# Kernel tuning notes

Measured on AMD Instinct MI355X. Metric: run time of the kernel, lower is better.

## Reference

```python
import jax, jax.numpy as jnp
import numpy as np

B, C, HIMG, WIMG = 32, 3, 512, 512


def setup_inputs() -> dict:
    key = jax.random.key(0)
    k1, k2, k3 = jax.random.split(key, 3)
    eye = jnp.eye(3, dtype=jnp.float32).reshape(1, 9)
    # near-identity homographies so inversion is well-conditioned
    H_pred = eye + 0.05 * jax.random.normal(k1, (B, 9), dtype=jnp.float32)
    H_true = eye + 0.05 * jax.random.normal(k2, (B, 9), dtype=jnp.float32)
    I = jax.random.normal(k3, (B, C, HIMG, WIMG), dtype=jnp.float32)
    return {"H_pred": H_pred, "H_true": H_true, "I": I}


def _build_perspective_grid(H_inv, height, width):
    # H_inv: [B,3,3] -> normalized sampling grid [B,height,width,2]
    xs = jnp.arange(width, dtype=jnp.float32)
    ys = jnp.arange(height, dtype=jnp.float32)
    gy, gx = jnp.meshgrid(ys, xs, indexing='ij')
    pts = jnp.stack([gx.ravel(), gy.ravel(), jnp.ones(height * width, dtype=jnp.float32)], axis=0)  # [3,N]
    new = jnp.einsum('bij,jn->bin', H_inv, pts)          # [B,3,N]
    new = new / new[:, 2:3, :]
    x_norm = 2.0 * new[:, 0] / (width - 1) - 1.0
    y_norm = 2.0 * new[:, 1] / (height - 1) - 1.0
    return jnp.stack([x_norm, y_norm], axis=-1).reshape(-1, height, width, 2)


def _grid_sample_bilinear_zeros(img, grid):
    # img: [B,C,H,W], grid: [B,H,W,2] in [-1,1]; align_corners=False, padding zeros
    Bn, Cn, Hn, Wn = img.shape
    x = ((grid[..., 0] + 1.0) * Wn - 1.0) * 0.5
    y = ((grid[..., 1] + 1.0) * Hn - 1.0) * 0.5
    x0 = jnp.floor(x); y0 = jnp.floor(y)
    x1 = x0 + 1.0;     y1 = y0 + 1.0
    wx1 = x - x0; wx0 = 1.0 - wx1
    wy1 = y - y0; wy0 = 1.0 - wy1

    def gather(xi, yi):
        valid = (xi >= 0) & (xi < Wn) & (yi >= 0) & (yi < Hn)
        xi_c = jnp.clip(xi, 0, Wn - 1).astype(jnp.int32)
        yi_c = jnp.clip(yi, 0, Hn - 1).astype(jnp.int32)
        vals = jax.vmap(lambda im, yy, xx: im[:, yy, xx])(img, yi_c, xi_c)  # [B,C,H,W]
        return vals * valid[:, None, :, :].astype(img.dtype)

    out = (gather(x0, y0) * (wx0 * wy0)[:, None]
           + gather(x1, y0) * (wx1 * wy0)[:, None]
           + gather(x0, y1) * (wx0 * wy1)[:, None]
           + gather(x1, y1) * (wx1 * wy1)[:, None])
    return out


def reference(H_pred, H_true, I):
    batch, _, h, w = I.shape
    Hp = H_pred.reshape(batch, 3, 3)
    Ht = H_true.reshape(batch, 3, 3)
    Hp_inv = jnp.linalg.inv(Hp)
    Ht_inv = jnp.linalg.inv(Ht)
    grid_pred = _build_perspective_grid(Hp_inv, h, w)
    grid_true = _build_perspective_grid(Ht_inv, h, w)
    I_pred = _grid_sample_bilinear_zeros(I, grid_pred)
    I_true = _grid_sample_bilinear_zeros(I, grid_true)
    return jnp.mean((I_pred - I_true) ** 2)
```

## Files before the change

kernel.cpp:

```cpp
#include <hip/hip_runtime.h>

#define IMG_B 32
#define IMG_C 3
#define IMG_H 512
#define IMG_W 512
#define HW_SHIFT 18
#define W_SHIFT 9

#define NBLOCKS_X IMG_H
#define NPARTIALS (NBLOCKS_X * IMG_B)

#define WS_INV_FLOATS (64 * 9)
#define WS_PART_OFFSET (WS_INV_FLOATS * sizeof(float))

__global__ void photoloss_invert_kernel(const float* __restrict__ Hp,
                                        const float* __restrict__ Ht,
                                        float* __restrict__ ws_inv) {
    int t = threadIdx.x;
    if (t < 64) {
        const float* src = (t < 32) ? (Hp + t * 9) : (Ht + (t - 32) * 9);
        float* dst = ws_inv + t * 9;
        double a = src[0], b = src[1], c = src[2];
        double d = src[3], e = src[4], f = src[5];
        double g = src[6], h = src[7], i = src[8];
        double A = e * i - f * h;
        double Bc = c * h - b * i;
        double Cc = b * f - c * e;
        double D = f * g - d * i;
        double E = a * i - c * g;
        double F = c * d - a * f;
        double G = d * h - e * g;
        double Hh = b * g - a * h;
        double Ii = a * e - b * d;
        double idet = 1.0 / (a * A + b * D + c * G);
        const double sc = (double)IMG_W / (double)(IMG_W - 1);
        dst[0] = (float)(A * idet * sc);
        dst[1] = (float)(Bc * idet * sc);
        dst[2] = (float)(Cc * idet * sc);
        dst[3] = (float)(D * idet * sc);
        dst[4] = (float)(E * idet * sc);
        dst[5] = (float)(F * idet * sc);
        dst[6] = (float)(G * idet);
        dst[7] = (float)(Hh * idet);
        dst[8] = (float)(Ii * idet);
    }
}

__device__ __forceinline__ void grid_setup_pair(float X, float Y, float Z,
                                                int* E, float* W) {
    const float iz = __builtin_amdgcn_rcpf(Z);
    const float xs = __builtin_fmaf(X, iz, -0.5f);
    const float ys = __builtin_fmaf(Y, iz, -0.5f);

    const float x0f = __builtin_floorf(xs);
    const float y0f = __builtin_floorf(ys);
    const int x0 = (int)x0f, y0 = (int)y0f;
    const int x1 = x0 + 1, y1 = y0 + 1;

    float wx1 = xs - x0f, wx0 = 1.0f - wx1;
    float wy1 = ys - y0f, wy0 = 1.0f - wy1;
    const float wx0m = ((unsigned)x0 < (unsigned)IMG_W) ? wx0 : 0.0f;
    const float wx1m = ((unsigned)x1 < (unsigned)IMG_W) ? wx1 : 0.0f;
    const float wy0m = ((unsigned)y0 < (unsigned)IMG_H) ? wy0 : 0.0f;
    const float wy1m = ((unsigned)y1 < (unsigned)IMG_H) ? wy1 : 0.0f;

    const bool sl = (x0 < 0);
    const float xA = sl ? wx1m : wx0m;
    const float xB = sl ? 0.0f : wx1m;
    const int xc0 = min(max(x0, 0), IMG_W - 1);

    const int e0r = y0 * IMG_W + xc0;
    const int e1r = e0r + IMG_W;
    const int emax = IMG_H * IMG_W - 2;
    const int e0 = min(max(e0r, 0), emax);
    const int e1 = min(max(e1r, 0), emax);
    const bool d0 = (e0 != e0r);
    const bool d1 = (e1 != e1r);
    const float uA0 = d0 ? 0.0f : xA, uB0 = d0 ? xA : xB;
    const float uA1 = d1 ? 0.0f : xA, uB1 = d1 ? xA : xB;

    E[0] = e0;
    E[1] = e1;
    W[0] = uA0 * wy0m; W[1] = uB0 * wy0m;
    W[2] = uA1 * wy1m; W[3] = uB1 * wy1m;
}

__device__ __forceinline__ float2 load_pair(const float* p) {
    float2 r;
    __builtin_memcpy(&r, p, 8);
    return r;
}

__global__ __launch_bounds__(256, 4) void photoloss_main_kernel(
        const float* __restrict__ I,
        const float* __restrict__ ws_inv,
        float* __restrict__ partials) {
    const int b = blockIdx.y;
    const int row = blockIdx.x;
    const int t = threadIdx.x;
    const float fy = (float)row;
    const float fx0 = (float)t;
    const float fx1 = (float)(t + 256);

    const float* __restrict__ hp = ws_inv + b * 9;
    const float* __restrict__ ht = ws_inv + (b + 32) * 9;

    const float cxp = __builtin_fmaf(hp[1], fy, hp[2]);
    const float cyp = __builtin_fmaf(hp[4], fy, hp[5]);
    const float czp = __builtin_fmaf(hp[7], fy, hp[8]);
    const float cxt = __builtin_fmaf(ht[1], fy, ht[2]);
    const float cyt = __builtin_fmaf(ht[4], fy, ht[5]);
    const float czt = __builtin_fmaf(ht[7], fy, ht[8]);

    int   Eoff[8];
    float W[16];
    grid_setup_pair(__builtin_fmaf(hp[0], fx0, cxp), __builtin_fmaf(hp[3], fx0, cyp),
                    __builtin_fmaf(hp[6], fx0, czp), Eoff + 0, W + 0);
    grid_setup_pair(__builtin_fmaf(ht[0], fx0, cxt), __builtin_fmaf(ht[3], fx0, cyt),
                    __builtin_fmaf(ht[6], fx0, czt), Eoff + 2, W + 4);
    grid_setup_pair(__builtin_fmaf(hp[0], fx1, cxp), __builtin_fmaf(hp[3], fx1, cyp),
                    __builtin_fmaf(hp[6], fx1, czp), Eoff + 4, W + 8);
    grid_setup_pair(__builtin_fmaf(ht[0], fx1, cxt), __builtin_fmaf(ht[3], fx1, cyt),
                    __builtin_fmaf(ht[6], fx1, czt), Eoff + 6, W + 12);

    bool pred[8];
#pragma unroll
    for (int k = 0; k < 8; ++k) {
        const int j = k >> 1, rr = k & 1;
        pred[k] = (W[4 * j + 2 * rr] + W[4 * j + 2 * rr + 1]) > 0.0f;
    }

    const float* __restrict__ ch0 = I + ((size_t)b * IMG_C << HW_SHIFT);
    const float* __restrict__ ch1 = ch0 + ((size_t)1 << HW_SHIFT);
    const float* __restrict__ ch2 = ch0 + ((size_t)2 << HW_SHIFT);

    float2 r[24];
#pragma unroll
    for (int k = 0; k < 8; ++k) {
        float2 v0 = make_float2(0.0f, 0.0f);
        float2 v1 = v0;
        float2 v2 = v0;
        if (pred[k]) {
            v0 = load_pair(ch0 + Eoff[k]);
            v1 = load_pair(ch1 + Eoff[k]);
            v2 = load_pair(ch2 + Eoff[k]);
        }
        r[0 * 8 + k] = v0;
        r[1 * 8 + k] = v1;
        r[2 * 8 + k] = v2;
    }

    float lsum = 0.0f;
#pragma unroll
    for (int c = 0; c < IMG_C; ++c) {
        const float2* rc = r + c * 8;
        const float sp0 = rc[0].x * W[0]  + rc[0].y * W[1]  + rc[1].x * W[2]  + rc[1].y * W[3];
        const float st0 = rc[2].x * W[4]  + rc[2].y * W[5]  + rc[3].x * W[6]  + rc[3].y * W[7];
        const float sp1 = rc[4].x * W[8]  + rc[4].y * W[9]  + rc[5].x * W[10] + rc[5].y * W[11];
        const float st1 = rc[6].x * W[12] + rc[6].y * W[13] + rc[7].x * W[14] + rc[7].y * W[15];
        const float d0 = sp0 - st0;
        const float d1 = sp1 - st1;
        lsum = __builtin_fmaf(d0, d0, lsum);
        lsum = __builtin_fmaf(d1, d1, lsum);
    }

#pragma unroll
    for (int off = 32; off > 0; off >>= 1)
        lsum += __shfl_down(lsum, off, 64);

    __shared__ float wsum[4];
    const int lane = threadIdx.x & 63;
    const int wid = threadIdx.x >> 6;
    if (lane == 0) wsum[wid] = lsum;
    __syncthreads();
    if (threadIdx.x == 0) {
        partials[blockIdx.y * gridDim.x + blockIdx.x] = wsum[0] + wsum[1] + wsum[2] + wsum[3];
    }
}

__global__ __launch_bounds__(1024) void photoloss_reduce_kernel(
        const float* __restrict__ partials, float* __restrict__ out) {
    double s = 0.0;
    for (int i = threadIdx.x; i < NPARTIALS; i += 1024)
        s += (double)partials[i];
#pragma unroll
    for (int off = 32; off > 0; off >>= 1)
        s += __shfl_down(s, off, 64);

    __shared__ double wsum[16];
    const int lane = threadIdx.x & 63;
    const int wid = threadIdx.x >> 6;
    if (lane == 0) wsum[wid] = s;
    __syncthreads();
    if (threadIdx.x == 0) {
        double total = 0.0;
#pragma unroll
        for (int i = 0; i < 16; ++i) total += wsum[i];
        const double n = (double)IMG_B * IMG_C * IMG_H * IMG_W;
        out[0] = (float)(total / n);
    }
}

extern "C" void kernel_launch(void* const* d_in, const int* in_sizes, int n_in,
                              void* d_out, int out_size, void* d_ws, size_t ws_size,
                              hipStream_t stream) {
    const float* Hp = (const float*)d_in[0];
    const float* Ht = (const float*)d_in[1];
    const float* I  = (const float*)d_in[2];
    float* out = (float*)d_out;

    float* ws_inv = (float*)d_ws;
    float* partials = (float*)((char*)d_ws + WS_PART_OFFSET);

    photoloss_invert_kernel<<<1, 64, 0, stream>>>(Hp, Ht, ws_inv);

    dim3 grid(NBLOCKS_X, IMG_B);
    photoloss_main_kernel<<<grid, 256, 0, stream>>>(I, ws_inv, partials);

    photoloss_reduce_kernel<<<1, 1024, 0, stream>>>(partials, out);
}
```

Before: 188.4 us.

## Process two rows per block and reuse shared source row between adjacent rows

Each block now handles two adjacent output rows instead of one, with a loop over the two 256-pixel column halves. When the bottom source row of output row A equals the top source row of output row B, that row's loads are skipped and the already-loaded values are reused, which cuts global gathers. It also halves the grid and the partial count. In exchange there are more live registers per iteration, extra predicate logic, and fewer blocks in flight.

```diff
diff --git a/kernel.cpp b/kernel.cpp
--- a/kernel.cpp
+++ b/kernel.cpp
@@ -7,7 +7,7 @@
 #define HW_SHIFT 18
 #define W_SHIFT 9
 
-#define NBLOCKS_X IMG_H
+#define NBLOCKS_X (IMG_H / 2)
 #define NPARTIALS (NBLOCKS_X * IMG_B)
 
 #define WS_INV_FLOATS (64 * 9)
@@ -96,72 +96,97 @@
         const float* __restrict__ ws_inv,
         float* __restrict__ partials) {
     const int b = blockIdx.y;
-    const int row = blockIdx.x;
+    const int r0 = blockIdx.x * 2;
     const int t = threadIdx.x;
-    const float fy = (float)row;
-    const float fx0 = (float)t;
-    const float fx1 = (float)(t + 256);
+    const float fyA = (float)r0;
+    const float fyB = (float)(r0 + 1);
 
     const float* __restrict__ hp = ws_inv + b * 9;
     const float* __restrict__ ht = ws_inv + (b + 32) * 9;
 
-    const float cxp = __builtin_fmaf(hp[1], fy, hp[2]);
-    const float cyp = __builtin_fmaf(hp[4], fy, hp[5]);
-    const float czp = __builtin_fmaf(hp[7], fy, hp[8]);
-    const float cxt = __builtin_fmaf(ht[1], fy, ht[2]);
-    const float cyt = __builtin_fmaf(ht[4], fy, ht[5]);
-    const float czt = __builtin_fmaf(ht[7], fy, ht[8]);
-
-    int   Eoff[8];
-    float W[16];
-    grid_setup_pair(__builtin_fmaf(hp[0], fx0, cxp), __builtin_fmaf(hp[3], fx0, cyp),
-                    __builtin_fmaf(hp[6], fx0, czp), Eoff + 0, W + 0);
-    grid_setup_pair(__builtin_fmaf(ht[0], fx0, cxt), __builtin_fmaf(ht[3], fx0, cyt),
-                    __builtin_fmaf(ht[6], fx0, czt), Eoff + 2, W + 4);
-    grid_setup_pair(__builtin_fmaf(hp[0], fx1, cxp), __builtin_fmaf(hp[3], fx1, cyp),
-                    __builtin_fmaf(hp[6], fx1, czp), Eoff + 4, W + 8);
-    grid_setup_pair(__builtin_fmaf(ht[0], fx1, cxt), __builtin_fmaf(ht[3], fx1, cyt),
-                    __builtin_fmaf(ht[6], fx1, czt), Eoff + 6, W + 12);
-
-    bool pred[8];
-#pragma unroll
-    for (int k = 0; k < 8; ++k) {
-        const int j = k >> 1, rr = k & 1;
-        pred[k] = (W[4 * j + 2 * rr] + W[4 * j + 2 * rr + 1]) > 0.0f;
-    }
+    const float cxpA = __builtin_fmaf(hp[1], fyA, hp[2]);
+    const float cypA = __builtin_fmaf(hp[4], fyA, hp[5]);
+    const float czpA = __builtin_fmaf(hp[7], fyA, hp[8]);
+    const float cxpB = __builtin_fmaf(hp[1], fyB, hp[2]);
+    const float cypB = __builtin_fmaf(hp[4], fyB, hp[5]);
+    const float czpB = __builtin_fmaf(hp[7], fyB, hp[8]);
+    const float cxtA = __builtin_fmaf(ht[1], fyA, ht[2]);
+    const float cytA = __builtin_fmaf(ht[4], fyA, ht[5]);
+    const float cztA = __builtin_fmaf(ht[7], fyA, ht[8]);
+    const float cxtB = __builtin_fmaf(ht[1], fyB, ht[2]);
+    const float cytB = __builtin_fmaf(ht[4], fyB, ht[5]);
+    const float cztB = __builtin_fmaf(ht[7], fyB, ht[8]);
+
+    const float hp0 = hp[0], hp3 = hp[3], hp6 = hp[6];
+    const float ht0 = ht[0], ht3 = ht[3], ht6 = ht[6];
 
     const float* __restrict__ ch0 = I + ((size_t)b * IMG_C << HW_SHIFT);
     const float* __restrict__ ch1 = ch0 + ((size_t)1 << HW_SHIFT);
     const float* __restrict__ ch2 = ch0 + ((size_t)2 << HW_SHIFT);
 
-    float2 r[24];
-#pragma unroll
-    for (int k = 0; k < 8; ++k) {
-        float2 v0 = make_float2(0.0f, 0.0f);
-        float2 v1 = v0;
-        float2 v2 = v0;
-        if (pred[k]) {
-            v0 = load_pair(ch0 + Eoff[k]);
-            v1 = load_pair(ch1 + Eoff[k]);
-            v2 = load_pair(ch2 + Eoff[k]);
+    float lsum = 0.0f;
+
+    for (int cc = 0; cc < 2; ++cc) {
+        const float fx = (float)(t + (cc << 8));
+
+        int E[8];
+        float Wc[16];
+        grid_setup_pair(__builtin_fmaf(hp0, fx, cxpA), __builtin_fmaf(hp3, fx, cypA),
+                        __builtin_fmaf(hp6, fx, czpA), E + 0, Wc + 0);
+        grid_setup_pair(__builtin_fmaf(hp0, fx, cxpB), __builtin_fmaf(hp3, fx, cypB),
+                        __builtin_fmaf(hp6, fx, czpB), E + 2, Wc + 4);
+        grid_setup_pair(__builtin_fmaf(ht0, fx, cxtA), __builtin_fmaf(ht3, fx, cytA),
+                        __builtin_fmaf(ht6, fx, cztA), E + 4, Wc + 8);
+        grid_setup_pair(__builtin_fmaf(ht0, fx, cxtB), __builtin_fmaf(ht3, fx, cytB),
+                        __builtin_fmaf(ht6, fx, cztB), E + 6, Wc + 12);
+
+        const bool shp = (E[2] == E[1]);
+        const bool sht = (E[6] == E[5]);
+
+        float ps[8];
+#pragma unroll
+        for (int k = 0; k < 8; ++k) ps[k] = Wc[2 * k] + Wc[2 * k + 1];
+
+        bool pr[8];
+        pr[0] = ps[0] > 0.0f;
+        pr[1] = (ps[1] > 0.0f) || (shp && (ps[2] > 0.0f));
+        pr[2] = (ps[2] > 0.0f) && !shp;
+        pr[3] = ps[3] > 0.0f;
+        pr[4] = ps[4] > 0.0f;
+        pr[5] = (ps[5] > 0.0f) || (sht && (ps[6] > 0.0f));
+        pr[6] = (ps[6] > 0.0f) && !sht;
+        pr[7] = ps[7] > 0.0f;
+
+        float2 r[24];
+#pragma unroll
+        for (int j = 0; j < 8; ++j) {
+            float2 v0 = make_float2(0.0f, 0.0f);
+            float2 v1 = v0;
+            float2 v2 = v0;
+            if (pr[j]) {
+                v0 = load_pair(ch0 + E[j]);
+                v1 = load_pair(ch1 + E[j]);
+                v2 = load_pair(ch2 + E[j]);
+            }
+            r[0 * 8 + j] = v0;
+            r[1 * 8 + j] = v1;
+            r[2 * 8 + j] = v2;
         }
-        r[0 * 8 + k] = v0;
-        r[1 * 8 + k] = v1;
-        r[2 * 8 + k] = v2;
-    }
-
-    float lsum = 0.0f;
-#pragma unroll
-    for (int c = 0; c < IMG_C; ++c) {
-        const float2* rc = r + c * 8;
-        const float sp0 = rc[0].x * W[0]  + rc[0].y * W[1]  + rc[1].x * W[2]  + rc[1].y * W[3];
-        const float st0 = rc[2].x * W[4]  + rc[2].y * W[5]  + rc[3].x * W[6]  + rc[3].y * W[7];
-        const float sp1 = rc[4].x * W[8]  + rc[4].y * W[9]  + rc[5].x * W[10] + rc[5].y * W[11];
-        const float st1 = rc[6].x * W[12] + rc[6].y * W[13] + rc[7].x * W[14] + rc[7].y * W[15];
-        const float d0 = sp0 - st0;
-        const float d1 = sp1 - st1;
-        lsum = __builtin_fmaf(d0, d0, lsum);
-        lsum = __builtin_fmaf(d1, d1, lsum);
+
+#pragma unroll
+        for (int c = 0; c < IMG_C; ++c) {
+            const float2* rc = r + c * 8;
+            const float2 pb0 = shp ? rc[1] : rc[2];
+            const float2 tb0 = sht ? rc[5] : rc[6];
+            const float spA = rc[0].x * Wc[0]  + rc[0].y * Wc[1]  + rc[1].x * Wc[2]  + rc[1].y * Wc[3];
+            const float spB = pb0.x   * Wc[4]  + pb0.y   * Wc[5]  + rc[3].x * Wc[6]  + rc[3].y * Wc[7];
+            const float stA = rc[4].x * Wc[8]  + rc[4].y * Wc[9]  + rc[5].x * Wc[10] + rc[5].y * Wc[11];
+            const float stB = tb0.x   * Wc[12] + tb0.y   * Wc[13] + rc[7].x * Wc[14] + rc[7].y * Wc[15];
+            const float dA = spA - stA;
+            const float dB = spB - stB;
+            lsum = __builtin_fmaf(dA, dA, lsum);
+            lsum = __builtin_fmaf(dB, dB, lsum);
+        }
     }
 
 #pragma unroll
```

Measured after the change: 232.2 us. 23.2% more time.
